# Kernel optimization log

Hardware: AMD Instinct MI355X
Metric: run time of the kernel (lower is better)

The kernel has to match this reference:

```python
import jax, jax.numpy as jnp
import numpy as np

DIM = 64
CTX_DIM = 128
B, D, H, W = 4, 64, 64, 64


def setup_inputs() -> dict:
    key = jax.random.key(0)
    ks = jax.random.split(key, 8)
    s_x = 1.0 / np.sqrt(DIM)
    s_c = 1.0 / np.sqrt(CTX_DIM)
    return {
        "x": jax.random.normal(ks[0], (B, DIM, D, H, W), dtype=jnp.float32),
        "context": jax.random.normal(ks[1], (B, CTX_DIM, D, H, W), dtype=jnp.float32),
        # 1x1x1 Conv3d weights flattened to [out_ch, in_ch] plus bias [out_ch]
        "wq": jax.random.uniform(ks[2], (DIM, DIM), jnp.float32, -s_x, s_x),
        "bq": jax.random.uniform(ks[3], (DIM,), jnp.float32, -s_x, s_x),
        "wk": jax.random.uniform(ks[4], (DIM, CTX_DIM), jnp.float32, -s_c, s_c),
        "bk": jax.random.uniform(ks[5], (DIM,), jnp.float32, -s_c, s_c),
        "wv": jax.random.uniform(ks[6], (DIM, CTX_DIM), jnp.float32, -s_c, s_c),
        "bv": jax.random.uniform(ks[7], (DIM,), jnp.float32, -s_c, s_c),
    }


def reference(x, context, wq, bq, wk, bk, wv, bv):
    # 1x1x1 Conv3d == per-voxel channel GEMM
    def conv1(w, b, t):
        return jnp.einsum('oc,bcdhw->bodhw', w, t) + b[None, :, None, None, None]

    scale = x.shape[1] ** (-0.5)
    q = conv1(wq, bq, x)          # [B, dim, D, H, W]
    k = conv1(wk, bk, context)    # [B, dim, D, H, W]
    v = conv1(wv, bv, context)    # [B, dim, D, H, W]

    # (q*scale) @ k^T batched over (B, dim, D): [H,W] @ [W,H] -> [H,H]
    attn = jnp.einsum('bcdhw,bcdgw->bcdhg', q * scale, k)  # [B, dim, D, H, H]
    attn = jax.nn.softmax(attn, axis=-1)
    out = jnp.einsum('bcdhg,bcdgw->bcdhw', attn, v)        # [B, dim, D, H, W]
    return out + x
```

## Files before the change

kernel.cpp:

```cpp
#include <hip/hip_runtime.h>
#include <hip/hip_bf16.h>

typedef short short8 __attribute__((ext_vector_type(8)));
typedef float floatx4 __attribute__((ext_vector_type(4)));
typedef unsigned short ushort_t;

#define NB   4
#define NC_X 64
#define NC_C 128
#define ND   64
#define NHW  4096
#define NH   64
#define NW   64

__device__ __forceinline__ ushort_t f2bf(float f) {
    unsigned u;
    __builtin_memcpy(&u, &f, 4);
    u += 0x7fffu + ((u >> 16) & 1u);
    return (ushort_t)(u >> 16);
}

__global__ void prep_kernel(const float* __restrict__ wq, const float* __restrict__ bq,
                            const float* __restrict__ wk, const float* __restrict__ bk,
                            const float* __restrict__ wv, const float* __restrict__ bv,
                            ushort_t* __restrict__ wW, float* __restrict__ wB) {
    int t = blockIdx.x * blockDim.x + threadIdx.x;
    int N = gridDim.x * blockDim.x;
    for (int i = t; i < 4096; i += N) wW[i] = f2bf(wq[i] * 0.125f);
    for (int i = t; i < 8192; i += N) wW[4096 + i] = f2bf(wk[i]);
    for (int i = t; i < 8192; i += N) wW[12288 + i] = f2bf(wv[i]);
    for (int i = t; i < 64; i += N) {
        wB[i] = bq[i] * 0.125f;
        wB[64 + i] = bk[i];
        wB[128 + i] = bv[i];
    }
}

__global__ __launch_bounds__(256, 2)
void proj_kernel(const float* __restrict__ x, const float* __restrict__ ctx,
                 const ushort_t* __restrict__ wW, const float* __restrict__ wB,
                 ushort_t* __restrict__ qws, ushort_t* __restrict__ kws,
                 ushort_t* __restrict__ vws, int b, int d0, int nd) {
    __shared__ ushort_t Xs[128][72];
    __shared__ ushort_t Cs[128][136];

    const int t = threadIdx.x;
    const int chunk = blockIdx.x;
    const int dd = blockIdx.y;
    const int d = d0 + dd;
    const int hw0 = chunk * 128;

    const float* xb = x + ((size_t)(b * NC_X) * ND + d) * NHW + hw0;
    const float* cb = ctx + ((size_t)(b * NC_C) * ND + d) * NHW + hw0;

    {
        const int hw = t & 127;
        const int icg0 = (t >> 7) * 4;
        #pragma unroll
        for (int i = 0; i < 4; ++i) {
            const int ic = (icg0 + i) * 8;
            short8 v;
            #pragma unroll
            for (int j = 0; j < 8; ++j)
                v[j] = (short)f2bf(xb[(size_t)(ic + j) * (ND * NHW) + hw]);
            *(short8*)&Xs[hw][ic] = v;
        }
        const int icg0c = (t >> 7) * 8;
        #pragma unroll
        for (int i = 0; i < 8; ++i) {
            const int ic = (icg0c + i) * 8;
            short8 v;
            #pragma unroll
            for (int j = 0; j < 8; ++j)
                v[j] = (short)f2bf(cb[(size_t)(ic + j) * (ND * NHW) + hw]);
            *(short8*)&Cs[hw][ic] = v;
        }
    }
    __syncthreads();

    const int wv = t >> 6, lane = t & 63, l15 = lane & 15, quad = lane >> 4;
    const floatx4 zero4 = {0.f, 0.f, 0.f, 0.f};

    short8 aQ[4][2];
    #pragma unroll
    for (int mt = 0; mt < 4; ++mt)
        #pragma unroll
        for (int kk = 0; kk < 2; ++kk)
            aQ[mt][kk] = *(const short8*)&wW[(mt * 16 + l15) * 64 + kk * 32 + quad * 8];

    floatx4 acc[4][2];
    #pragma unroll
    for (int mt = 0; mt < 4; ++mt)
        #pragma unroll
        for (int n = 0; n < 2; ++n) acc[mt][n] = zero4;

    #pragma unroll
    for (int kk = 0; kk < 2; ++kk) {
        short8 bX[2];
        #pragma unroll
        for (int n = 0; n < 2; ++n)
            bX[n] = *(const short8*)&Xs[(2 * wv + n) * 16 + l15][kk * 32 + quad * 8];
        #pragma unroll
        for (int mt = 0; mt < 4; ++mt)
            #pragma unroll
            for (int n = 0; n < 2; ++n)
                acc[mt][n] = __builtin_amdgcn_mfma_f32_16x16x32_bf16(
                    aQ[mt][kk], bX[n], acc[mt][n], 0, 0, 0);
    }
    #pragma unroll
    for (int mt = 0; mt < 4; ++mt)
        #pragma unroll
        for (int n = 0; n < 2; ++n) {
            const int col = hw0 + (2 * wv + n) * 16 + l15;
            #pragma unroll
            for (int r = 0; r < 4; ++r) {
                const int oc = mt * 16 + quad * 4 + r;
                qws[((size_t)(oc * nd + dd)) * NHW + col] = f2bf(acc[mt][n][r] + wB[oc]);
            }
        }

    floatx4 acc2[8][2];
    #pragma unroll
    for (int mt = 0; mt < 8; ++mt)
        #pragma unroll
        for (int n = 0; n < 2; ++n) acc2[mt][n] = zero4;

    #pragma unroll
    for (int kk = 0; kk < 4; ++kk) {
        short8 bC[2];
        #pragma unroll
        for (int n = 0; n < 2; ++n)
            bC[n] = *(const short8*)&Cs[(2 * wv + n) * 16 + l15][kk * 32 + quad * 8];
        #pragma unroll
        for (int mt = 0; mt < 8; ++mt) {
            const short8 aW =
                *(const short8*)&wW[4096 + (mt * 16 + l15) * 128 + kk * 32 + quad * 8];
            #pragma unroll
            for (int n = 0; n < 2; ++n)
                acc2[mt][n] = __builtin_amdgcn_mfma_f32_16x16x32_bf16(
                    aW, bC[n], acc2[mt][n], 0, 0, 0);
        }
    }
    #pragma unroll
    for (int mt = 0; mt < 8; ++mt)
        #pragma unroll
        for (int n = 0; n < 2; ++n) {
            const int col = hw0 + (2 * wv + n) * 16 + l15;
            #pragma unroll
            for (int r = 0; r < 4; ++r) {
                const int row = mt * 16 + quad * 4 + r;
                const float val = acc2[mt][n][r] + wB[64 + row];
                ushort_t* dst = (row < 64) ? kws : vws;
                dst[((size_t)((row & 63) * nd + dd)) * NHW + col] = f2bf(val);
            }
        }
}

__global__ __launch_bounds__(256, 2)
void attn_kernel(const ushort_t* __restrict__ qws, const ushort_t* __restrict__ kws,
                 const ushort_t* __restrict__ vws, const float* __restrict__ x,
                 float* __restrict__ out, int b, int d0, int nd) {
    __shared__ ushort_t Vs[64][72];
    __shared__ ushort_t Ps[64][72];

    const int c = blockIdx.x, dd = blockIdx.y;
    const int d = d0 + dd;
    const ushort_t* qp = qws + (size_t)(c * nd + dd) * NHW;
    const ushort_t* kp = kws + (size_t)(c * nd + dd) * NHW;
    const ushort_t* vp = vws + (size_t)(c * nd + dd) * NHW;
    const float* xp = x + ((size_t)(b * NC_X + c) * ND + d) * NHW;
    float* op = out + ((size_t)(b * NC_X + c) * ND + d) * NHW;

    const int t = threadIdx.x;
    {
        const int w = t & 63;
        const int gg0 = (t >> 6) * 2;
        #pragma unroll
        for (int i = 0; i < 2; ++i) {
            const int g = (gg0 + i) * 8;
            short8 vvv;
            #pragma unroll
            for (int j = 0; j < 8; ++j) vvv[j] = (short)vp[(g + j) * NW + w];
            *(short8*)&Vs[w][g] = vvv;
        }
    }
    __syncthreads();

    const int wv = t >> 6, lane = t & 63, l15 = lane & 15, quad = lane >> 4;
    const floatx4 zero4 = {0.f, 0.f, 0.f, 0.f};

    short8 aQ[2], bK[4][2];
    #pragma unroll
    for (int kk = 0; kk < 2; ++kk)
        aQ[kk] = *(const short8*)&qp[(wv * 16 + l15) * NW + kk * 32 + quad * 8];
    #pragma unroll
    for (int nt = 0; nt < 4; ++nt)
        #pragma unroll
        for (int kk = 0; kk < 2; ++kk)
            bK[nt][kk] = *(const short8*)&kp[(nt * 16 + l15) * NW + kk * 32 + quad * 8];

    floatx4 s[4];
    #pragma unroll
    for (int nt = 0; nt < 4; ++nt) s[nt] = zero4;
    #pragma unroll
    for (int kk = 0; kk < 2; ++kk)
        #pragma unroll
        for (int nt = 0; nt < 4; ++nt)
            s[nt] = __builtin_amdgcn_mfma_f32_16x16x32_bf16(aQ[kk], bK[nt][kk], s[nt], 0, 0, 0);

    float linv[4];
    #pragma unroll
    for (int r = 0; r < 4; ++r) {
        float m = s[0][r];
        #pragma unroll
        for (int nt = 1; nt < 4; ++nt) m = fmaxf(m, s[nt][r]);
        #pragma unroll
        for (int off = 1; off < 16; off <<= 1) m = fmaxf(m, __shfl_xor(m, off, 64));
        float e[4], sum = 0.f;
        #pragma unroll
        for (int nt = 0; nt < 4; ++nt) {
            e[nt] = __expf(s[nt][r] - m);
            sum += e[nt];
        }
        #pragma unroll
        for (int off = 1; off < 16; off <<= 1) sum += __shfl_xor(sum, off, 64);
        linv[r] = 1.0f / sum;
        const int row = wv * 16 + quad * 4 + r;
        #pragma unroll
        for (int nt = 0; nt < 4; ++nt) Ps[row][nt * 16 + l15] = f2bf(e[nt]);
    }
    __syncthreads();

    short8 aP[2], bV[4][2];
    #pragma unroll
    for (int kk = 0; kk < 2; ++kk)
        aP[kk] = *(const short8*)&Ps[wv * 16 + l15][kk * 32 + quad * 8];
    #pragma unroll
    for (int nt = 0; nt < 4; ++nt)
        #pragma unroll
        for (int kk = 0; kk < 2; ++kk)
            bV[nt][kk] = *(const short8*)&Vs[nt * 16 + l15][kk * 32 + quad * 8];

    floatx4 o[4];
    #pragma unroll
    for (int nt = 0; nt < 4; ++nt) o[nt] = zero4;
    #pragma unroll
    for (int kk = 0; kk < 2; ++kk)
        #pragma unroll
        for (int nt = 0; nt < 4; ++nt)
            o[nt] = __builtin_amdgcn_mfma_f32_16x16x32_bf16(aP[kk], bV[nt][kk], o[nt], 0, 0, 0);

    #pragma unroll
    for (int nt = 0; nt < 4; ++nt)
        #pragma unroll
        for (int r = 0; r < 4; ++r) {
            const int row = wv * 16 + quad * 4 + r;
            const int col = nt * 16 + l15;
            op[row * NW + col] = o[nt][r] * linv[r] + xp[row * NW + col];
        }
}

extern "C" void kernel_launch(void* const* d_in, const int* in_sizes, int n_in,
                              void* d_out, int out_size, void* d_ws, size_t ws_size,
                              hipStream_t stream) {
    const float* x = (const float*)d_in[0];
    const float* ctx = (const float*)d_in[1];
    const float* wq = (const float*)d_in[2];
    const float* bq = (const float*)d_in[3];
    const float* wk = (const float*)d_in[4];
    const float* bk = (const float*)d_in[5];
    const float* wv = (const float*)d_in[6];
    const float* bv = (const float*)d_in[7];
    float* out = (float*)d_out;

    ushort_t* wW = (ushort_t*)d_ws;
    float* wB = (float*)((char*)d_ws + 40960);

    const size_t perD = 3ull * NC_X * NHW * 2;
    size_t avail = (ws_size > 65536) ? ws_size - 65536 : perD;
    int DS = (int)(avail / perD);
    if (DS > ND) DS = ND;
    if (DS < 1) DS = 1;

    ushort_t* qws = (ushort_t*)((char*)d_ws + 65536);
    ushort_t* kws = qws + (size_t)NC_X * DS * NHW;
    ushort_t* vws = kws + (size_t)NC_X * DS * NHW;

    prep_kernel<<<dim3(32), dim3(256), 0, stream>>>(wq, bq, wk, bk, wv, bv, wW, wB);

    for (int b = 0; b < NB; ++b) {
        for (int d0 = 0; d0 < ND; d0 += DS) {
            const int nd = (ND - d0 < DS) ? (ND - d0) : DS;
            proj_kernel<<<dim3(32, nd), dim3(256), 0, stream>>>(
                x, ctx, wW, wB, qws, kws, vws, b, d0, nd);
            attn_kernel<<<dim3(64, nd), dim3(256), 0, stream>>>(
                qws, kws, vws, x, out, b, d0, nd);
        }
    }
}
```

Measured before the change: 1.262 ms.

## Flatten batch/depth into slice windows, prefetch residual, raise attn occupancy

Merges the batch and depth loops into one flat slice index so each launch pair can span batch boundaries, using fewer and larger launches when the workspace allows. The attention kernel now loads the residual x values into registers at the start so the global load latency overlaps the V staging and the matmuls. Its launch bounds go from 2 to 3 blocks per SM, which lowers the register budget and may cause spills because the prefetched x values add registers.

```diff
diff --git a/kernel.cpp b/kernel.cpp
--- a/kernel.cpp
+++ b/kernel.cpp
@@ -12,6 +12,7 @@
 #define NHW  4096
 #define NH   64
 #define NW   64
+#define NS   (NB * ND)
 
 __device__ __forceinline__ ushort_t f2bf(float f) {
     unsigned u;
@@ -40,14 +41,16 @@
 void proj_kernel(const float* __restrict__ x, const float* __restrict__ ctx,
                  const ushort_t* __restrict__ wW, const float* __restrict__ wB,
                  ushort_t* __restrict__ qws, ushort_t* __restrict__ kws,
-                 ushort_t* __restrict__ vws, int b, int d0, int nd) {
+                 ushort_t* __restrict__ vws, int s0, int nd) {
     __shared__ ushort_t Xs[128][72];
     __shared__ ushort_t Cs[128][136];
 
     const int t = threadIdx.x;
     const int chunk = blockIdx.x;
-    const int dd = blockIdx.y;
-    const int d = d0 + dd;
+    const int si = blockIdx.y;
+    const int s = s0 + si;
+    const int b = s >> 6;
+    const int d = s & 63;
     const int hw0 = chunk * 128;
 
     const float* xb = x + ((size_t)(b * NC_X) * ND + d) * NHW + hw0;
@@ -115,7 +118,7 @@
             #pragma unroll
             for (int r = 0; r < 4; ++r) {
                 const int oc = mt * 16 + quad * 4 + r;
-                qws[((size_t)(oc * nd + dd)) * NHW + col] = f2bf(acc[mt][n][r] + wB[oc]);
+                qws[((size_t)(oc * nd + si)) * NHW + col] = f2bf(acc[mt][n][r] + wB[oc]);
             }
         }
 
@@ -151,27 +154,38 @@
                 const int row = mt * 16 + quad * 4 + r;
                 const float val = acc2[mt][n][r] + wB[64 + row];
                 ushort_t* dst = (row < 64) ? kws : vws;
-                dst[((size_t)((row & 63) * nd + dd)) * NHW + col] = f2bf(val);
+                dst[((size_t)((row & 63) * nd + si)) * NHW + col] = f2bf(val);
             }
         }
 }
 
-__global__ __launch_bounds__(256, 2)
+__global__ __launch_bounds__(256, 3)
 void attn_kernel(const ushort_t* __restrict__ qws, const ushort_t* __restrict__ kws,
                  const ushort_t* __restrict__ vws, const float* __restrict__ x,
-                 float* __restrict__ out, int b, int d0, int nd) {
+                 float* __restrict__ out, int s0, int nd) {
     __shared__ ushort_t Vs[64][72];
     __shared__ ushort_t Ps[64][72];
 
-    const int c = blockIdx.x, dd = blockIdx.y;
-    const int d = d0 + dd;
-    const ushort_t* qp = qws + (size_t)(c * nd + dd) * NHW;
-    const ushort_t* kp = kws + (size_t)(c * nd + dd) * NHW;
-    const ushort_t* vp = vws + (size_t)(c * nd + dd) * NHW;
+    const int c = blockIdx.x, si = blockIdx.y;
+    const int s = s0 + si;
+    const int b = s >> 6;
+    const int d = s & 63;
+    const ushort_t* qp = qws + (size_t)(c * nd + si) * NHW;
+    const ushort_t* kp = kws + (size_t)(c * nd + si) * NHW;
+    const ushort_t* vp = vws + (size_t)(c * nd + si) * NHW;
     const float* xp = x + ((size_t)(b * NC_X + c) * ND + d) * NHW;
     float* op = out + ((size_t)(b * NC_X + c) * ND + d) * NHW;
 
     const int t = threadIdx.x;
+    const int wv = t >> 6, lane = t & 63, l15 = lane & 15, quad = lane >> 4;
+
+    float xv[4][4];
+    #pragma unroll
+    for (int nt = 0; nt < 4; ++nt)
+        #pragma unroll
+        for (int r = 0; r < 4; ++r)
+            xv[nt][r] = xp[(wv * 16 + quad * 4 + r) * NW + nt * 16 + l15];
+
     {
         const int w = t & 63;
         const int gg0 = (t >> 6) * 2;
@@ -186,7 +200,6 @@
     }
     __syncthreads();
 
-    const int wv = t >> 6, lane = t & 63, l15 = lane & 15, quad = lane >> 4;
     const floatx4 zero4 = {0.f, 0.f, 0.f, 0.f};
 
     short8 aQ[2], bK[4][2];
@@ -199,27 +212,27 @@
         for (int kk = 0; kk < 2; ++kk)
             bK[nt][kk] = *(const short8*)&kp[(nt * 16 + l15) * NW + kk * 32 + quad * 8];
 
-    floatx4 s[4];
-    #pragma unroll
-    for (int nt = 0; nt < 4; ++nt) s[nt] = zero4;
+    floatx4 sA[4];
+    #pragma unroll
+    for (int nt = 0; nt < 4; ++nt) sA[nt] = zero4;
     #pragma unroll
     for (int kk = 0; kk < 2; ++kk)
         #pragma unroll
         for (int nt = 0; nt < 4; ++nt)
-            s[nt] = __builtin_amdgcn_mfma_f32_16x16x32_bf16(aQ[kk], bK[nt][kk], s[nt], 0, 0, 0);
+            sA[nt] = __builtin_amdgcn_mfma_f32_16x16x32_bf16(aQ[kk], bK[nt][kk], sA[nt], 0, 0, 0);
 
     float linv[4];
     #pragma unroll
     for (int r = 0; r < 4; ++r) {
-        float m = s[0][r];
-        #pragma unroll
-        for (int nt = 1; nt < 4; ++nt) m = fmaxf(m, s[nt][r]);
+        float m = sA[0][r];
+        #pragma unroll
+        for (int nt = 1; nt < 4; ++nt) m = fmaxf(m, sA[nt][r]);
         #pragma unroll
         for (int off = 1; off < 16; off <<= 1) m = fmaxf(m, __shfl_xor(m, off, 64));
         float e[4], sum = 0.f;
         #pragma unroll
         for (int nt = 0; nt < 4; ++nt) {
-            e[nt] = __expf(s[nt][r] - m);
+            e[nt] = __expf(sA[nt][r] - m);
             sum += e[nt];
         }
         #pragma unroll
@@ -256,7 +269,7 @@
         for (int r = 0; r < 4; ++r) {
             const int row = wv * 16 + quad * 4 + r;
             const int col = nt * 16 + l15;
-            op[row * NW + col] = o[nt][r] * linv[r] + xp[row * NW + col];
+            op[row * NW + col] = o[nt][r] * linv[r] + xv[nt][r];
         }
 }
 
@@ -276,25 +289,23 @@
     ushort_t* wW = (ushort_t*)d_ws;
     float* wB = (float*)((char*)d_ws + 40960);
 
-    const size_t perD = 3ull * NC_X * NHW * 2;
-    size_t avail = (ws_size > 65536) ? ws_size - 65536 : perD;
-    int DS = (int)(avail / perD);
-    if (DS > ND) DS = ND;
-    if (DS < 1) DS = 1;
+    const size_t perSlice = 3ull * NC_X * NHW * 2;
+    size_t avail = (ws_size > 65536) ? ws_size - 65536 : perSlice;
+    int W = (int)(avail / perSlice);
+    if (W > NS) W = NS;
+    if (W < 1) W = 1;
 
     ushort_t* qws = (ushort_t*)((char*)d_ws + 65536);
-    ushort_t* kws = qws + (size_t)NC_X * DS * NHW;
-    ushort_t* vws = kws + (size_t)NC_X * DS * NHW;
+    ushort_t* kws = qws + (size_t)NC_X * W * NHW;
+    ushort_t* vws = kws + (size_t)NC_X * W * NHW;
 
     prep_kernel<<<dim3(32), dim3(256), 0, stream>>>(wq, bq, wk, bk, wv, bv, wW, wB);
 
-    for (int b = 0; b < NB; ++b) {
-        for (int d0 = 0; d0 < ND; d0 += DS) {
-            const int nd = (ND - d0 < DS) ? (ND - d0) : DS;
-            proj_kernel<<<dim3(32, nd), dim3(256), 0, stream>>>(
-                x, ctx, wW, wB, qws, kws, vws, b, d0, nd);
-            attn_kernel<<<dim3(64, nd), dim3(256), 0, stream>>>(
-                qws, kws, vws, x, out, b, d0, nd);
-        }
-    }
-}
+    for (int s0 = 0; s0 < NS; s0 += W) {
+        const int w = (NS - s0 < W) ? (NS - s0) : W;
+        proj_kernel<<<dim3(32, w), dim3(256), 0, stream>>>(
+            x, ctx, wW, wB, qws, kws, vws, s0, w);
+        attn_kernel<<<dim3(64, w), dim3(256), 0, stream>>>(
+            qws, kws, vws, x, out, s0, w);
+    }
+}
```

Result: no change. 1.238 ms (-1.9%).
